# Kernel optimization log

Hardware: AMD Instinct MI355X
Metric: run time of the kernel (lower is better)

The kernel has to match this reference:

```python
import jax, jax.numpy as jnp
import numpy as np

TIME_STEPS = 100
SPIKE_THRESHOLD = 0.5
INPUT_DIM = 8192


def setup_inputs() -> dict:
    key = jax.random.key(0)
    k_x, k_w = jax.random.split(key)
    x = jax.random.uniform(k_x, (INPUT_DIM,), dtype=jnp.float32)
    # matches nn.Parameter(torch.rand(D, D) * 0.01)
    synaptic_weights = jax.random.uniform(k_w, (INPUT_DIM, INPUT_DIM), dtype=jnp.float32) * 0.01
    # matches nn.Parameter(torch.zeros(D))
    membrane_potential = jnp.zeros((INPUT_DIM,), dtype=jnp.float32)
    return {"x": x, "synaptic_weights": synaptic_weights, "membrane_potential": membrane_potential}


def reference(x, synaptic_weights, membrane_potential):
    # Drive is identical every timestep (x and W are loop-invariant), so compute once.
    drive = x @ synaptic_weights  # [D]

    def step(pot, _):
        pot = pot + drive
        spike = (pot >= SPIKE_THRESHOLD).astype(pot.dtype)  # spike_mask.float()
        pot = pot * (1.0 - spike)  # membrane_potential[spike_mask] = 0
        return pot, (spike, pot)

    _, (spikes, potentials) = jax.lax.scan(step, membrane_potential, None, length=TIME_STEPS)
    synaptic_activity = jnp.abs(synaptic_weights).mean()
    # spikes: [T, D], potentials: [T, D], synaptic_activity: scalar
    return spikes, potentials, synaptic_activity
```

## Files before the change

### kernel.cpp

```cpp
#include <hip/hip_runtime.h>

#define D 8192
#define T_STEPS 100
#define SPIKE_THR 0.5f
#define BLOCK 256
#define COLS_PER_THREAD 4
#define NCHUNK 256
#define ROWS_PER_CHUNK (D / NCHUNK)
#define COLBLOCKS (D / (BLOCK * COLS_PER_THREAD))
#define STEPS_PER 4
#define TCHUNKS (T_STEPS / STEPS_PER)
#define RED_COLS 64
#define RED_SEGS (BLOCK / RED_COLS)
#define RED_BLOCKS (D / RED_COLS)

__global__ void __launch_bounds__(BLOCK)
k_partial(const float* __restrict__ x, const float* __restrict__ W,
          float* __restrict__ ws_drive, float* __restrict__ ws_abs) {
    __shared__ float xs[ROWS_PER_CHUNK];
    __shared__ float red[BLOCK];

    const int chunk = blockIdx.y;
    const int row0  = chunk * ROWS_PER_CHUNK;
    if (threadIdx.x < ROWS_PER_CHUNK)
        xs[threadIdx.x] = x[row0 + threadIdx.x];
    __syncthreads();

    const int j0 = (blockIdx.x * BLOCK + threadIdx.x) * COLS_PER_THREAD;

    float ax = 0.f, ay = 0.f, az = 0.f, aw = 0.f;
    float asum = 0.f;
    #pragma unroll 8
    for (int i = 0; i < ROWS_PER_CHUNK; ++i) {
        const float xv = xs[i];
        const float4 w = *reinterpret_cast<const float4*>(
            &W[(size_t)(row0 + i) * D + j0]);
        ax = fmaf(xv, w.x, ax);
        ay = fmaf(xv, w.y, ay);
        az = fmaf(xv, w.z, az);
        aw = fmaf(xv, w.w, aw);
        asum += fabsf(w.x) + fabsf(w.y) + fabsf(w.z) + fabsf(w.w);
    }

    float4 acc; acc.x = ax; acc.y = ay; acc.z = az; acc.w = aw;
    *reinterpret_cast<float4*>(&ws_drive[(size_t)chunk * D + j0]) = acc;

    red[threadIdx.x] = asum;
    __syncthreads();
    for (int s = BLOCK / 2; s > 0; s >>= 1) {
        if (threadIdx.x < s) red[threadIdx.x] += red[threadIdx.x + s];
        __syncthreads();
    }
    if (threadIdx.x == 0)
        ws_abs[blockIdx.y * gridDim.x + blockIdx.x] = red[0];
}

__global__ void __launch_bounds__(BLOCK)
k_reduce(const float* __restrict__ ws_drive, const float* __restrict__ ws_abs,
         float* __restrict__ drive, float* __restrict__ out) {
    if (blockIdx.x == RED_BLOCKS) {
        __shared__ float red[BLOCK];
        const int n = NCHUNK * COLBLOCKS;
        float s = 0.f;
        for (int i = threadIdx.x; i < n; i += BLOCK) s += ws_abs[i];
        red[threadIdx.x] = s;
        __syncthreads();
        for (int st = BLOCK / 2; st > 0; st >>= 1) {
            if (threadIdx.x < st) red[threadIdx.x] += red[threadIdx.x + st];
            __syncthreads();
        }
        if (threadIdx.x == 0)
            out[(size_t)2 * T_STEPS * D] = red[0] / ((float)D * (float)D);
        return;
    }

    __shared__ float part[RED_SEGS][RED_COLS];
    const int col = threadIdx.x & (RED_COLS - 1);
    const int seg = threadIdx.x >> 6;
    const int j   = blockIdx.x * RED_COLS + col;

    float s = 0.f;
    const int c0 = seg * (NCHUNK / RED_SEGS);
    #pragma unroll 8
    for (int cc = 0; cc < NCHUNK / RED_SEGS; ++cc)
        s += ws_drive[(size_t)(c0 + cc) * D + j];
    part[seg][col] = s;
    __syncthreads();
    if (seg == 0)
        drive[j] = part[0][col] + part[1][col] + part[2][col] + part[3][col];
}

__global__ void __launch_bounds__(BLOCK)
k_sim(const float* __restrict__ drive, const float* __restrict__ pot0,
      float* __restrict__ out) {
    const int j0 = (blockIdx.x * BLOCK + threadIdx.x) * COLS_PER_THREAD;
    const int t0 = blockIdx.y * STEPS_PER;

    const float4 d  = *reinterpret_cast<const float4*>(&drive[j0]);
    const float4 p0 = *reinterpret_cast<const float4*>(&pot0[j0]);
    float px = p0.x, py = p0.y, pz = p0.z, pw = p0.w;

    for (int t = 0; t < t0; ++t) {
        px += d.x; py += d.y; pz += d.z; pw += d.w;
        px = (px >= SPIKE_THR) ? 0.f : px;
        py = (py >= SPIKE_THR) ? 0.f : py;
        pz = (pz >= SPIKE_THR) ? 0.f : pz;
        pw = (pw >= SPIKE_THR) ? 0.f : pw;
    }

    float* __restrict__ spikes = out;
    float* __restrict__ pots   = out + (size_t)T_STEPS * D;

    #pragma unroll
    for (int s = 0; s < STEPS_PER; ++s) {
        const int t = t0 + s;
        px += d.x; py += d.y; pz += d.z; pw += d.w;
        float4 sp;
        sp.x = (px >= SPIKE_THR) ? 1.f : 0.f;
        sp.y = (py >= SPIKE_THR) ? 1.f : 0.f;
        sp.z = (pz >= SPIKE_THR) ? 1.f : 0.f;
        sp.w = (pw >= SPIKE_THR) ? 1.f : 0.f;
        px *= (1.f - sp.x); py *= (1.f - sp.y);
        pz *= (1.f - sp.z); pw *= (1.f - sp.w);
        *reinterpret_cast<float4*>(&spikes[(size_t)t * D + j0]) = sp;
        float4 pv; pv.x = px; pv.y = py; pv.z = pz; pv.w = pw;
        *reinterpret_cast<float4*>(&pots[(size_t)t * D + j0]) = pv;
    }
}

extern "C" void kernel_launch(void* const* d_in, const int* in_sizes, int n_in,
                              void* d_out, int out_size, void* d_ws, size_t ws_size,
                              hipStream_t stream) {
    const float* x   = (const float*)d_in[0];
    const float* W   = (const float*)d_in[1];
    const float* mp0 = (const float*)d_in[2];
    float* out = (float*)d_out;

    float* ws_drive = (float*)d_ws;
    float* ws_abs   = ws_drive + (size_t)NCHUNK * D;
    float* drive    = ws_abs + NCHUNK * COLBLOCKS;

    dim3 g1(COLBLOCKS, NCHUNK);
    k_partial<<<g1, BLOCK, 0, stream>>>(x, W, ws_drive, ws_abs);
    k_reduce<<<RED_BLOCKS + 1, BLOCK, 0, stream>>>(ws_drive, ws_abs, drive, out);
    dim3 g3(COLBLOCKS, TCHUNKS);
    k_sim<<<g3, BLOCK, 0, stream>>>(drive, mp0, out);
}
```

Measured before the change: 58.56 us.

## Fuse drive reduction with spike simulation and use nontemporal weight loads

Merges the reduce and simulation kernels into one: each reduce block computes the drive for its 64 columns in shared memory, and each of its 4 thread segments then simulates and writes 25 timesteps for those columns. This removes one kernel launch and the global round-trip of the drive vector. Weight loads in the partial GEMV now use nontemporal loads so the streamed matrix does not pollute the cache. In exchange, the sim stage runs on only 129 blocks with scalar stores and longer serial per-thread work, which may leave the output-write phase underparallelized.

```diff
diff --git a/kernel.cpp b/kernel.cpp
--- a/kernel.cpp
+++ b/kernel.cpp
@@ -8,11 +8,12 @@
 #define NCHUNK 256
 #define ROWS_PER_CHUNK (D / NCHUNK)
 #define COLBLOCKS (D / (BLOCK * COLS_PER_THREAD))
-#define STEPS_PER 4
-#define TCHUNKS (T_STEPS / STEPS_PER)
 #define RED_COLS 64
 #define RED_SEGS (BLOCK / RED_COLS)
 #define RED_BLOCKS (D / RED_COLS)
+#define STEPS_PER_SEG (T_STEPS / RED_SEGS)
+
+typedef float f32x4 __attribute__((ext_vector_type(4)));
 
 __global__ void __launch_bounds__(BLOCK)
 k_partial(const float* __restrict__ x, const float* __restrict__ W,
@@ -33,8 +34,8 @@
     #pragma unroll 8
     for (int i = 0; i < ROWS_PER_CHUNK; ++i) {
         const float xv = xs[i];
-        const float4 w = *reinterpret_cast<const float4*>(
-            &W[(size_t)(row0 + i) * D + j0]);
+        const f32x4 w = __builtin_nontemporal_load(
+            reinterpret_cast<const f32x4*>(&W[(size_t)(row0 + i) * D + j0]));
         ax = fmaf(xv, w.x, ax);
         ay = fmaf(xv, w.y, ay);
         az = fmaf(xv, w.z, az);
@@ -56,8 +57,8 @@
 }
 
 __global__ void __launch_bounds__(BLOCK)
-k_reduce(const float* __restrict__ ws_drive, const float* __restrict__ ws_abs,
-         float* __restrict__ drive, float* __restrict__ out) {
+k_fused(const float* __restrict__ ws_drive, const float* __restrict__ ws_abs,
+        const float* __restrict__ pot0, float* __restrict__ out) {
     if (blockIdx.x == RED_BLOCKS) {
         __shared__ float red[BLOCK];
         const int n = NCHUNK * COLBLOCKS;
@@ -86,45 +87,27 @@
         s += ws_drive[(size_t)(c0 + cc) * D + j];
     part[seg][col] = s;
     __syncthreads();
-    if (seg == 0)
-        drive[j] = part[0][col] + part[1][col] + part[2][col] + part[3][col];
-}
 
-__global__ void __launch_bounds__(BLOCK)
-k_sim(const float* __restrict__ drive, const float* __restrict__ pot0,
-      float* __restrict__ out) {
-    const int j0 = (blockIdx.x * BLOCK + threadIdx.x) * COLS_PER_THREAD;
-    const int t0 = blockIdx.y * STEPS_PER;
+    const float d = part[0][col] + part[1][col] + part[2][col] + part[3][col];
+    float p = pot0[j];
 
-    const float4 d  = *reinterpret_cast<const float4*>(&drive[j0]);
-    const float4 p0 = *reinterpret_cast<const float4*>(&pot0[j0]);
-    float px = p0.x, py = p0.y, pz = p0.z, pw = p0.w;
-
+    const int t0 = seg * STEPS_PER_SEG;
     for (int t = 0; t < t0; ++t) {
-        px += d.x; py += d.y; pz += d.z; pw += d.w;
-        px = (px >= SPIKE_THR) ? 0.f : px;
-        py = (py >= SPIKE_THR) ? 0.f : py;
-        pz = (pz >= SPIKE_THR) ? 0.f : pz;
-        pw = (pw >= SPIKE_THR) ? 0.f : pw;
+        p += d;
+        p = (p >= SPIKE_THR) ? 0.f : p;
     }
 
     float* __restrict__ spikes = out;
     float* __restrict__ pots   = out + (size_t)T_STEPS * D;
 
     #pragma unroll
-    for (int s = 0; s < STEPS_PER; ++s) {
-        const int t = t0 + s;
-        px += d.x; py += d.y; pz += d.z; pw += d.w;
-        float4 sp;
-        sp.x = (px >= SPIKE_THR) ? 1.f : 0.f;
-        sp.y = (py >= SPIKE_THR) ? 1.f : 0.f;
-        sp.z = (pz >= SPIKE_THR) ? 1.f : 0.f;
-        sp.w = (pw >= SPIKE_THR) ? 1.f : 0.f;
-        px *= (1.f - sp.x); py *= (1.f - sp.y);
-        pz *= (1.f - sp.z); pw *= (1.f - sp.w);
-        *reinterpret_cast<float4*>(&spikes[(size_t)t * D + j0]) = sp;
-        float4 pv; pv.x = px; pv.y = py; pv.z = pz; pv.w = pw;
-        *reinterpret_cast<float4*>(&pots[(size_t)t * D + j0]) = pv;
+    for (int s2 = 0; s2 < STEPS_PER_SEG; ++s2) {
+        const int t = t0 + s2;
+        p += d;
+        const float sp = (p >= SPIKE_THR) ? 1.f : 0.f;
+        p *= (1.f - sp);
+        spikes[(size_t)t * D + j] = sp;
+        pots[(size_t)t * D + j]   = p;
     }
 }
 
@@ -138,11 +121,8 @@
 
     float* ws_drive = (float*)d_ws;
     float* ws_abs   = ws_drive + (size_t)NCHUNK * D;
-    float* drive    = ws_abs + NCHUNK * COLBLOCKS;
 
     dim3 g1(COLBLOCKS, NCHUNK);
     k_partial<<<g1, BLOCK, 0, stream>>>(x, W, ws_drive, ws_abs);
-    k_reduce<<<RED_BLOCKS + 1, BLOCK, 0, stream>>>(ws_drive, ws_abs, drive, out);
-    dim3 g3(COLBLOCKS, TCHUNKS);
-    k_sim<<<g3, BLOCK, 0, stream>>>(drive, mp0, out);
+    k_fused<<<RED_BLOCKS + 1, BLOCK, 0, stream>>>(ws_drive, ws_abs, mp0, out);
 }
```

Result: slower. 64.24 us (+9.7%).
